# Optimization experiments

Hardware: AMD Instinct MI355X
Metric: run time of the kernel (lower is better)

Reference implementation:

```python
import jax, jax.numpy as jnp
import numpy as np

B, LX, LM, D = 4, 512, 512, 256

def setup_inputs() -> dict:
    key = jax.random.key(0)
    ks = jax.random.split(key, 7)
    s = 1.0 / np.sqrt(D)
    return {
        "x": jax.random.normal(ks[0], (B, LX, D), jnp.float32),
        "memory": jax.random.normal(ks[1], (B, LM, D), jnp.float32),
        "memory_mask": jax.random.randint(ks[2], (B, LM), 0, 2, jnp.int32),
        "W1": jax.random.normal(ks[3], (D, D), jnp.float32) * s,
        "b1": jax.random.normal(ks[4], (D,), jnp.float32) * s,
        "W2": jax.random.normal(ks[5], (D, D), jnp.float32) * s,
        "Wt": jax.random.normal(ks[6], (D,), jnp.float32) * s,
    }

def reference(x, memory, memory_mask, W1, b1, W2, Wt):
    # item1: (B, Lx, D); item2: (B, Lm, D)
    item1 = jnp.einsum("bxd,ed->bxe", x, W1) + b1
    item2 = jnp.einsum("bmd,ed->bme", memory, W2)
    # additive attention: tanh of broadcast sum, then reduce D to scalar logit
    item = item1[:, :, None, :] + item2[:, None, :, :]  # (B, Lx, Lm, D)
    S_logit = jnp.einsum("bxmd,d->bxm", jnp.tanh(item), Wt)
    S_logit = jnp.where(memory_mask[:, None, :] == 0, jnp.float32(-10000.0), S_logit)
    return S_logit
```

## Files before the change

### kernel.cpp

```cpp
#include <hip/hip_runtime.h>

namespace {

constexpr int B = 4, LX = 512, LM = 512, D = 256;
constexpr float KSCALE = 2.8853900817779268f;
constexpr float CLAMP = 7.5f;

typedef __attribute__((ext_vector_type(8))) short short8;
typedef __attribute__((ext_vector_type(4))) float f32x4;
typedef __attribute__((ext_vector_type(2))) float f32x2;

__device__ __forceinline__ unsigned bfbits(float f) {
    unsigned u = __float_as_uint(f);
    u += 0x7FFFu + ((u >> 16) & 1u);
    return u >> 16;
}
__device__ __forceinline__ int pack2(float a, float b) {
    return (int)(bfbits(a) | (bfbits(b) << 16));
}
__device__ __forceinline__ f32x2 up2(unsigned u) {
    f32x2 r;
    r.x = __uint_as_float(u << 16);
    r.y = __uint_as_float(u & 0xFFFF0000u);
    return r;
}

__global__ __launch_bounds__(256) void proj_mfma(
    const float* __restrict__ x, const float* __restrict__ mem,
    const float* __restrict__ W1, const float* __restrict__ b1v,
    const float* __restrict__ W2,
    unsigned short* __restrict__ E1h, unsigned short* __restrict__ E2h)
{
    const int tid = threadIdx.x;
    const int m0c = blockIdx.x * 32;
    const int e0  = blockIdx.y * 64;
    const int z   = m0c >= 2048;
    const int r0  = z ? (m0c - 2048) : m0c;
    const float* __restrict__ A = (z ? mem : x) + (size_t)r0 * D;
    const float* __restrict__ W = z ? W2 : W1;
    unsigned short* __restrict__ Eh = z ? E2h : E1h;

    __shared__ short sA[32][40];
    __shared__ short sW[64][40];

    const int wv = tid >> 6, lane = tid & 63;
    const int lr = lane & 15, quad = lane >> 4;
    const int g   = wv & 1;
    const int cg0 = (wv >> 1) * 2;
    const int srA = tid >> 3;
    const int scA = (tid & 7) * 4;

    f32x4 acc0 = {0.f, 0.f, 0.f, 0.f};
    f32x4 acc1 = {0.f, 0.f, 0.f, 0.f};

    for (int kc = 0; kc < D; kc += 32) {
        float4 av = *(const float4*)&A[(size_t)srA * D + kc + scA];
        float4 w0 = *(const float4*)&W[(size_t)(e0 + srA) * D + kc + scA];
        float4 w1 = *(const float4*)&W[(size_t)(e0 + 32 + srA) * D + kc + scA];
        __syncthreads();
        *(int2*)&sA[srA][scA]      = make_int2(pack2(av.x, av.y), pack2(av.z, av.w));
        *(int2*)&sW[srA][scA]      = make_int2(pack2(w0.x, w0.y), pack2(w0.z, w0.w));
        *(int2*)&sW[srA + 32][scA] = make_int2(pack2(w1.x, w1.y), pack2(w1.z, w1.w));
        __syncthreads();
        short8 af  = *(const short8*)&sA[g * 16 + lr][quad * 8];
        short8 bf0 = *(const short8*)&sW[cg0 * 16 + lr][quad * 8];
        short8 bf1 = *(const short8*)&sW[cg0 * 16 + 16 + lr][quad * 8];
        acc0 = __builtin_amdgcn_mfma_f32_16x16x32_bf16(af, bf0, acc0, 0, 0, 0);
        acc1 = __builtin_amdgcn_mfma_f32_16x16x32_bf16(af, bf1, acc1, 0, 0, 0);
    }

    const float bias0 = z ? 0.f : b1v[e0 + cg0 * 16 + lr];
    const float bias1 = z ? 0.f : b1v[e0 + cg0 * 16 + 16 + lr];
    const int ec0 = e0 + cg0 * 16 + lr;
#pragma unroll
    for (int reg = 0; reg < 4; ++reg) {
        const int pair = quad * 4 + reg;
        const size_t base = (size_t)((r0 >> 5) * 16 + pair) * 256;
        float a0 = KSCALE * (acc0[reg] + bias0);
        float a1 = KSCALE * (acc1[reg] + bias1);
        a0 = fminf(fmaxf(a0, -CLAMP), CLAMP);
        a1 = fminf(fmaxf(a1, -CLAMP), CLAMP);
        Eh[(base + ec0) * 2 + g] =
            (unsigned short)bfbits(__builtin_amdgcn_exp2f(a0));
        Eh[(base + ec0 + 16) * 2 + g] =
            (unsigned short)bfbits(__builtin_amdgcn_exp2f(a1));
    }
}

__global__ __launch_bounds__(256) void tanh_score_kernel(
    const unsigned* __restrict__ E1p, const unsigned* __restrict__ E2p,
    const float* __restrict__ Wt, const int* __restrict__ mask,
    float* __restrict__ out)
{
    const int tid = threadIdx.x;
    const int b  = blockIdx.z;
    const int x0 = blockIdx.y * 32;
    const int m0 = blockIdx.x * 64;
    const int xt = (b * LX + x0) >> 5;
    const int mt = (b * LM + m0) >> 5;

    __shared__ unsigned sA[16 * 132];
    __shared__ unsigned sB[32 * 132];

    const int tx = tid & 15, ty = tid >> 4;
    const int pA = tid >> 4, cA = (tid & 15) * 4;
    const int rB = tid >> 3, cB = (tid & 7) * 4;
    const unsigned* gA = E1p + (size_t)(xt * 16 + pA) * 256;
    const unsigned* gB = E2p + (size_t)((mt + (rB >> 4)) * 16 + (rB & 15)) * 256;

    float sumW = 0.f;
#pragma unroll
    for (int i = 0; i < 256; i += 4) {
        const float4 w = *(const float4*)&Wt[i];
        sumW += (w.x + w.y) + (w.z + w.w);
    }

    f32x2 acc01s = {0.f, 0.f}, acc01w = {0.f, 0.f};
    f32x2 acc23s = {0.f, 0.f}, acc23w = {0.f, 0.f};
    const f32x2 one2 = {1.f, 1.f};

    for (int c = 0; c < 2; ++c) {
        const int dB = c * 128;
        uint4 A0 = *(const uint4*)(gA + dB + cA);
        uint4 A1 = *(const uint4*)(gA + dB + 64 + cA);
        uint4 B0 = *(const uint4*)(gB + dB + cB);
        uint4 B1 = *(const uint4*)(gB + dB + 32 + cB);
        uint4 B2 = *(const uint4*)(gB + dB + 64 + cB);
        uint4 B3 = *(const uint4*)(gB + dB + 96 + cB);
        __syncthreads();
        *(uint4*)&sA[pA * 132 + cA]      = A0;
        *(uint4*)&sA[pA * 132 + 64 + cA] = A1;
        *(uint4*)&sB[rB * 132 + cB]      = B0;
        *(uint4*)&sB[rB * 132 + 32 + cB] = B1;
        *(uint4*)&sB[rB * 132 + 64 + cB] = B2;
        *(uint4*)&sB[rB * 132 + 96 + cB] = B3;
        __syncthreads();

#pragma unroll 1
        for (int d = 0; d < 128; d += 8) {
            const uint4 ua0 = *(const uint4*)&sA[ty * 132 + d];
            const uint4 ua1 = *(const uint4*)&sA[ty * 132 + d + 4];
            const uint4 ub0 = *(const uint4*)&sB[tx * 132 + d];
            const uint4 ub1 = *(const uint4*)&sB[tx * 132 + d + 4];
            const uint4 uc0 = *(const uint4*)&sB[(16 + tx) * 132 + d];
            const uint4 uc1 = *(const uint4*)&sB[(16 + tx) * 132 + d + 4];
            const float4 w0 = *(const float4*)&Wt[dB + d];
            const float4 w1 = *(const float4*)&Wt[dB + d + 4];

            const f32x2 a_[8] = {up2(ua0.x), up2(ua0.y), up2(ua0.z), up2(ua0.w),
                                 up2(ua1.x), up2(ua1.y), up2(ua1.z), up2(ua1.w)};
            const f32x2 p_[8] = {up2(ub0.x), up2(ub0.y), up2(ub0.z), up2(ub0.w),
                                 up2(ub1.x), up2(ub1.y), up2(ub1.z), up2(ub1.w)};
            const f32x2 q_[8] = {up2(uc0.x), up2(uc0.y), up2(uc0.z), up2(uc0.w),
                                 up2(uc1.x), up2(uc1.y), up2(uc1.z), up2(uc1.w)};
            const float wv[8] = {w0.x, w0.y, w0.z, w0.w, w1.x, w1.y, w1.z, w1.w};

#define SPL(s)  ((f32x2){(s), (s)})
#define FMA2(A_, B_, C_) __builtin_elementwise_fma((A_), (B_), (C_))
#define OCT(BX, accv) { \
    const f32x2 T0 = FMA2(a_[0], BX(0), one2), T1 = FMA2(a_[1], BX(1), one2); \
    const f32x2 T2 = FMA2(a_[2], BX(2), one2), T3 = FMA2(a_[3], BX(3), one2); \
    const f32x2 T4 = FMA2(a_[4], BX(4), one2), T5 = FMA2(a_[5], BX(5), one2); \
    const f32x2 T6 = FMA2(a_[6], BX(6), one2), T7 = FMA2(a_[7], BX(7), one2); \
    const f32x2 L0 = T0 * T1, L1 = T2 * T3, L2 = T4 * T5, L3 = T6 * T7;       \
    const f32x2 Q0 = L0 * L1, Q1 = L2 * L3;                                   \
    const f32x2 den = Q0 * Q1;                                                \
    const f32x2 n0 = FMA2(SPL(wv[0]), T1, SPL(wv[1]) * T0);                   \
    const f32x2 n1 = FMA2(SPL(wv[2]), T3, SPL(wv[3]) * T2);                   \
    const f32x2 n2 = FMA2(SPL(wv[4]), T5, SPL(wv[5]) * T4);                   \
    const f32x2 n3 = FMA2(SPL(wv[6]), T7, SPL(wv[7]) * T6);                   \
    const f32x2 u0 = FMA2(n0, L1, n1 * L0), u1 = FMA2(n2, L3, n3 * L2);       \
    const f32x2 N  = FMA2(u0, Q1, u1 * Q0);                                   \
    f32x2 r; r.x = __builtin_amdgcn_rcpf(den.x);                              \
             r.y = __builtin_amdgcn_rcpf(den.y);                              \
    (accv) = FMA2(N, r, (accv)); }

#define BP(i)  (p_[i])
#define BPS(i) (__builtin_shufflevector(p_[i], p_[i], 1, 0))
#define BQ(i)  (q_[i])
#define BQS(i) (__builtin_shufflevector(q_[i], q_[i], 1, 0))
            OCT(BP,  acc01s)
            OCT(BPS, acc01w)
            OCT(BQ,  acc23s)
            OCT(BQS, acc23w)
#undef BP
#undef BPS
#undef BQ
#undef BQS
#undef OCT
#undef FMA2
#undef SPL
        }
    }

    const int xA = x0 + ty, xB = x0 + 16 + ty;
    const int mmv[4] = {m0 + tx, m0 + 16 + tx, m0 + 32 + tx, m0 + 48 + tx};
    const float vA[4] = {acc01s.x, acc01w.x, acc23s.x, acc23w.x};
    const float vB[4] = {acc01w.y, acc01s.y, acc23w.y, acc23s.y};
#pragma unroll
    for (int k = 0; k < 4; ++k) {
        const bool keep = mask[b * LM + mmv[k]] != 0;
        out[((size_t)b * LX + xA) * LM + mmv[k]] =
            keep ? (sumW - 2.f * vA[k]) : -10000.f;
        out[((size_t)b * LX + xB) * LM + mmv[k]] =
            keep ? (sumW - 2.f * vB[k]) : -10000.f;
    }
}

}

extern "C" void kernel_launch(void* const* d_in, const int* in_sizes, int n_in,
                              void* d_out, int out_size, void* d_ws, size_t ws_size,
                              hipStream_t stream)
{
    const float* x    = (const float*)d_in[0];
    const float* mem  = (const float*)d_in[1];
    const int*   mask = (const int*)d_in[2];
    const float* W1   = (const float*)d_in[3];
    const float* b1   = (const float*)d_in[4];
    const float* W2   = (const float*)d_in[5];
    const float* Wt   = (const float*)d_in[6];
    float* out = (float*)d_out;

    unsigned* E1p = (unsigned*)d_ws;
    unsigned* E2p = E1p + (size_t)(B * LX / 32) * 16 * 256;

    proj_mfma<<<dim3(128, 4), 256, 0, stream>>>(
        x, mem, W1, b1, W2, (unsigned short*)E1p, (unsigned short*)E2p);

    tanh_score_kernel<<<dim3(LM / 64, LX / 32, B), 256, 0, stream>>>(
        E1p, E2p, Wt, mask, out);
}
```

Baseline: 106.3 us.

## Skip masked memory columns via compacted index list and prefilled output

Adds a kernel that compacts the valid memory indices per batch, plus a kernel that pre-fills the output with -10000. The score kernel then computes tanh scores only for the compacted valid columns, gathering E2 rows in a new row-major layout and scattering results to their original columns. This removes the transcendental-heavy work for masked positions. In exchange it adds two launches, a full output fill pass, and gather/scatter indirection.

```diff
diff --git a/kernel.cpp b/kernel.cpp
--- a/kernel.cpp
+++ b/kernel.cpp
@@ -23,6 +23,9 @@
     r.x = __uint_as_float(u << 16);
     r.y = __uint_as_float(u & 0xFFFF0000u);
     return r;
+}
+__device__ __forceinline__ unsigned permb(unsigned hi, unsigned lo, unsigned sel) {
+    return __builtin_amdgcn_perm(hi, lo, sel);
 }
 
 __global__ __launch_bounds__(256) void proj_mfma(
@@ -38,7 +41,6 @@
     const int r0  = z ? (m0c - 2048) : m0c;
     const float* __restrict__ A = (z ? mem : x) + (size_t)r0 * D;
     const float* __restrict__ W = z ? W2 : W1;
-    unsigned short* __restrict__ Eh = z ? E2h : E1h;
 
     __shared__ short sA[32][40];
     __shared__ short sW[64][40];
@@ -75,38 +77,69 @@
 #pragma unroll
     for (int reg = 0; reg < 4; ++reg) {
         const int pair = quad * 4 + reg;
-        const size_t base = (size_t)((r0 >> 5) * 16 + pair) * 256;
         float a0 = KSCALE * (acc0[reg] + bias0);
         float a1 = KSCALE * (acc1[reg] + bias1);
         a0 = fminf(fmaxf(a0, -CLAMP), CLAMP);
         a1 = fminf(fmaxf(a1, -CLAMP), CLAMP);
-        Eh[(base + ec0) * 2 + g] =
-            (unsigned short)bfbits(__builtin_amdgcn_exp2f(a0));
-        Eh[(base + ec0 + 16) * 2 + g] =
-            (unsigned short)bfbits(__builtin_amdgcn_exp2f(a1));
-    }
+        const unsigned short e0b = (unsigned short)bfbits(__builtin_amdgcn_exp2f(a0));
+        const unsigned short e1b = (unsigned short)bfbits(__builtin_amdgcn_exp2f(a1));
+        if (!z) {
+            const size_t base = (size_t)((r0 >> 5) * 16 + pair) * 256;
+            E1h[(base + ec0) * 2 + g]      = e0b;
+            E1h[(base + ec0 + 16) * 2 + g] = e1b;
+        } else {
+            const int row = r0 + g * 16 + pair;
+            E2h[(size_t)row * 256 + ec0]      = e0b;
+            E2h[(size_t)row * 256 + ec0 + 16] = e1b;
+        }
+    }
+}
+
+__global__ __launch_bounds__(256) void compact_mask(
+    const int* __restrict__ mask, int* __restrict__ cidx, int* __restrict__ cnt)
+{
+    const int b    = threadIdx.x >> 6;
+    const int lane = threadIdx.x & 63;
+    int base = 0;
+    for (int c = 0; c < LM / 64; ++c) {
+        const int m = c * 64 + lane;
+        const bool bit = mask[b * LM + m] != 0;
+        const unsigned long long bal = __ballot(bit);
+        const int pre = __popcll(bal & ((1ull << lane) - 1ull));
+        if (bit) cidx[b * LM + base + pre] = m;
+        base += __popcll(bal);
+    }
+    if (lane == 0) cnt[b] = base;
+}
+
+__global__ __launch_bounds__(256) void fill_out_kernel(float4* __restrict__ out4)
+{
+    const int i = blockIdx.x * 256 + threadIdx.x;
+    const float4 v = make_float4(-10000.f, -10000.f, -10000.f, -10000.f);
+    out4[i]          = v;
+    out4[i + 131072] = v;
 }
 
 __global__ __launch_bounds__(256) void tanh_score_kernel(
-    const unsigned* __restrict__ E1p, const unsigned* __restrict__ E2p,
-    const float* __restrict__ Wt, const int* __restrict__ mask,
-    float* __restrict__ out)
+    const unsigned* __restrict__ E1p, const unsigned* __restrict__ E2u,
+    const float* __restrict__ Wt, const int* __restrict__ cidx,
+    const int* __restrict__ cnt, float* __restrict__ out)
 {
     const int tid = threadIdx.x;
-    const int b  = blockIdx.z;
-    const int x0 = blockIdx.y * 32;
-    const int m0 = blockIdx.x * 64;
-    const int xt = (b * LX + x0) >> 5;
-    const int mt = (b * LM + m0) >> 5;
+    const int b   = blockIdx.z;
+    const int x0  = blockIdx.y * 32;
+    const int bx  = blockIdx.x;
+    const int count = cnt[b];
+    const int xt  = (b * LX + x0) >> 5;
 
     __shared__ unsigned sA[16 * 132];
-    __shared__ unsigned sB[32 * 132];
+    __shared__ unsigned sB[16 * 132];
 
     const int tx = tid & 15, ty = tid >> 4;
-    const int pA = tid >> 4, cA = (tid & 15) * 4;
-    const int rB = tid >> 3, cB = (tid & 7) * 4;
+    const int pA = tid >> 4, cA = (tid & 15) * 8;
+    const int pB = tid >> 4, iB = (tid & 15);
+
     const unsigned* gA = E1p + (size_t)(xt * 16 + pA) * 256;
-    const unsigned* gB = E2p + (size_t)((mt + (rB >> 4)) * 16 + (rB & 15)) * 256;
 
     float sumW = 0.f;
 #pragma unroll
@@ -115,45 +148,7 @@
         sumW += (w.x + w.y) + (w.z + w.w);
     }
 
-    f32x2 acc01s = {0.f, 0.f}, acc01w = {0.f, 0.f};
-    f32x2 acc23s = {0.f, 0.f}, acc23w = {0.f, 0.f};
     const f32x2 one2 = {1.f, 1.f};
-
-    for (int c = 0; c < 2; ++c) {
-        const int dB = c * 128;
-        uint4 A0 = *(const uint4*)(gA + dB + cA);
-        uint4 A1 = *(const uint4*)(gA + dB + 64 + cA);
-        uint4 B0 = *(const uint4*)(gB + dB + cB);
-        uint4 B1 = *(const uint4*)(gB + dB + 32 + cB);
-        uint4 B2 = *(const uint4*)(gB + dB + 64 + cB);
-        uint4 B3 = *(const uint4*)(gB + dB + 96 + cB);
-        __syncthreads();
-        *(uint4*)&sA[pA * 132 + cA]      = A0;
-        *(uint4*)&sA[pA * 132 + 64 + cA] = A1;
-        *(uint4*)&sB[rB * 132 + cB]      = B0;
-        *(uint4*)&sB[rB * 132 + 32 + cB] = B1;
-        *(uint4*)&sB[rB * 132 + 64 + cB] = B2;
-        *(uint4*)&sB[rB * 132 + 96 + cB] = B3;
-        __syncthreads();
-
-#pragma unroll 1
-        for (int d = 0; d < 128; d += 8) {
-            const uint4 ua0 = *(const uint4*)&sA[ty * 132 + d];
-            const uint4 ua1 = *(const uint4*)&sA[ty * 132 + d + 4];
-            const uint4 ub0 = *(const uint4*)&sB[tx * 132 + d];
-            const uint4 ub1 = *(const uint4*)&sB[tx * 132 + d + 4];
-            const uint4 uc0 = *(const uint4*)&sB[(16 + tx) * 132 + d];
-            const uint4 uc1 = *(const uint4*)&sB[(16 + tx) * 132 + d + 4];
-            const float4 w0 = *(const float4*)&Wt[dB + d];
-            const float4 w1 = *(const float4*)&Wt[dB + d + 4];
-
-            const f32x2 a_[8] = {up2(ua0.x), up2(ua0.y), up2(ua0.z), up2(ua0.w),
-                                 up2(ua1.x), up2(ua1.y), up2(ua1.z), up2(ua1.w)};
-            const f32x2 p_[8] = {up2(ub0.x), up2(ub0.y), up2(ub0.z), up2(ub0.w),
-                                 up2(ub1.x), up2(ub1.y), up2(ub1.z), up2(ub1.w)};
-            const f32x2 q_[8] = {up2(uc0.x), up2(uc0.y), up2(uc0.z), up2(uc0.w),
-                                 up2(uc1.x), up2(uc1.y), up2(uc1.z), up2(uc1.w)};
-            const float wv[8] = {w0.x, w0.y, w0.z, w0.w, w1.x, w1.y, w1.z, w1.w};
 
 #define SPL(s)  ((f32x2){(s), (s)})
 #define FMA2(A_, B_, C_) __builtin_elementwise_fma((A_), (B_), (C_))
@@ -174,37 +169,76 @@
     f32x2 r; r.x = __builtin_amdgcn_rcpf(den.x);                              \
              r.y = __builtin_amdgcn_rcpf(den.y);                              \
     (accv) = FMA2(N, r, (accv)); }
-
 #define BP(i)  (p_[i])
 #define BPS(i) (__builtin_shufflevector(p_[i], p_[i], 1, 0))
-#define BQ(i)  (q_[i])
-#define BQS(i) (__builtin_shufflevector(q_[i], q_[i], 1, 0))
-            OCT(BP,  acc01s)
-            OCT(BPS, acc01w)
-            OCT(BQ,  acc23s)
-            OCT(BQS, acc23w)
+
+    for (int s = bx; s < 16; s += 8) {
+        const int m0 = s * 32;
+        if (m0 >= count) break;
+
+        const int c_lo = min(m0 + pB, count - 1);
+        const int c_hi = min(m0 + pB + 16, count - 1);
+        const unsigned* rlo = E2u + (size_t)cidx[b * LM + c_lo] * 128;
+        const unsigned* rhi = E2u + (size_t)cidx[b * LM + c_hi] * 128;
+
+        f32x2 accs = {0.f, 0.f}, accw = {0.f, 0.f};
+
+        for (int c = 0; c < 2; ++c) {
+            const int dB = c * 128;
+            const uint4 A0 = *(const uint4*)(gA + dB + cA);
+            const uint4 A1 = *(const uint4*)(gA + dB + cA + 4);
+            const uint4 Lo = *(const uint4*)(rlo + c * 64 + iB * 4);
+            const uint4 Hi = *(const uint4*)(rhi + c * 64 + iB * 4);
+            uint4 P0, P1;
+            P0.x = permb(Hi.x, Lo.x, 0x05040100u); P0.y = permb(Hi.x, Lo.x, 0x07060302u);
+            P0.z = permb(Hi.y, Lo.y, 0x05040100u); P0.w = permb(Hi.y, Lo.y, 0x07060302u);
+            P1.x = permb(Hi.z, Lo.z, 0x05040100u); P1.y = permb(Hi.z, Lo.z, 0x07060302u);
+            P1.z = permb(Hi.w, Lo.w, 0x05040100u); P1.w = permb(Hi.w, Lo.w, 0x07060302u);
+            __syncthreads();
+            *(uint4*)&sA[pA * 132 + cA]         = A0;
+            *(uint4*)&sA[pA * 132 + cA + 4]     = A1;
+            *(uint4*)&sB[pB * 132 + iB * 8]     = P0;
+            *(uint4*)&sB[pB * 132 + iB * 8 + 4] = P1;
+            __syncthreads();
+
+#pragma unroll 1
+            for (int d = 0; d < 128; d += 8) {
+                const uint4 ua0 = *(const uint4*)&sA[ty * 132 + d];
+                const uint4 ua1 = *(const uint4*)&sA[ty * 132 + d + 4];
+                const uint4 ub0 = *(const uint4*)&sB[tx * 132 + d];
+                const uint4 ub1 = *(const uint4*)&sB[tx * 132 + d + 4];
+                const float4 w0 = *(const float4*)&Wt[dB + d];
+                const float4 w1 = *(const float4*)&Wt[dB + d + 4];
+
+                const f32x2 a_[8] = {up2(ua0.x), up2(ua0.y), up2(ua0.z), up2(ua0.w),
+                                     up2(ua1.x), up2(ua1.y), up2(ua1.z), up2(ua1.w)};
+                const f32x2 p_[8] = {up2(ub0.x), up2(ub0.y), up2(ub0.z), up2(ub0.w),
+                                     up2(ub1.x), up2(ub1.y), up2(ub1.z), up2(ub1.w)};
+                const float wv[8] = {w0.x, w0.y, w0.z, w0.w, w1.x, w1.y, w1.z, w1.w};
+
+                OCT(BP,  accs)
+                OCT(BPS, accw)
+            }
+        }
+
+        const int col0 = m0 + tx, col1 = m0 + 16 + tx;
+        const int xA = x0 + ty, xB = x0 + 16 + ty;
+        if (col0 < count) {
+            const int mo = cidx[b * LM + col0];
+            out[((size_t)b * LX + xA) * LM + mo] = sumW - 2.f * accs.x;
+            out[((size_t)b * LX + xB) * LM + mo] = sumW - 2.f * accw.y;
+        }
+        if (col1 < count) {
+            const int mo = cidx[b * LM + col1];
+            out[((size_t)b * LX + xA) * LM + mo] = sumW - 2.f * accw.x;
+            out[((size_t)b * LX + xB) * LM + mo] = sumW - 2.f * accs.y;
+        }
+    }
 #undef BP
 #undef BPS
-#undef BQ
-#undef BQS
 #undef OCT
 #undef FMA2
 #undef SPL
-        }
-    }
-
-    const int xA = x0 + ty, xB = x0 + 16 + ty;
-    const int mmv[4] = {m0 + tx, m0 + 16 + tx, m0 + 32 + tx, m0 + 48 + tx};
-    const float vA[4] = {acc01s.x, acc01w.x, acc23s.x, acc23w.x};
-    const float vB[4] = {acc01w.y, acc01s.y, acc23w.y, acc23s.y};
-#pragma unroll
-    for (int k = 0; k < 4; ++k) {
-        const bool keep = mask[b * LM + mmv[k]] != 0;
-        out[((size_t)b * LX + xA) * LM + mmv[k]] =
-            keep ? (sumW - 2.f * vA[k]) : -10000.f;
-        out[((size_t)b * LX + xB) * LM + mmv[k]] =
-            keep ? (sumW - 2.f * vB[k]) : -10000.f;
-    }
 }
 
 }
@@ -222,12 +256,15 @@
     const float* Wt   = (const float*)d_in[6];
     float* out = (float*)d_out;
 
-    unsigned* E1p = (unsigned*)d_ws;
-    unsigned* E2p = E1p + (size_t)(B * LX / 32) * 16 * 256;
-
+    unsigned*       E1p = (unsigned*)d_ws;
+    unsigned short* E2h = (unsigned short*)(E1p + (size_t)(B * LX / 32) * 16 * 256);
+    int* cidx = (int*)((char*)d_ws + 2u * 1024u * 1024u);
+    int* cnt  = cidx + B * LM;
+
+    fill_out_kernel<<<512, 256, 0, stream>>>((float4*)out);
+    compact_mask<<<1, 256, 0, stream>>>(mask, cidx, cnt);
     proj_mfma<<<dim3(128, 4), 256, 0, stream>>>(
-        x, mem, W1, b1, W2, (unsigned short*)E1p, (unsigned short*)E2p);
-
-    tanh_score_kernel<<<dim3(LM / 64, LX / 32, B), 256, 0, stream>>>(
-        E1p, E2p, Wt, mask, out);
-}
+        x, mem, W1, b1, W2, (unsigned short*)E1p, E2h);
+    tanh_score_kernel<<<dim3(8, 16, 4), 256, 0, stream>>>(
+        E1p, (const unsigned*)E2h, Wt, cidx, cnt, out);
+}
```

Result: no change. 105.7 us (-0.6%).
